# Kernel tuning notes

Hardware: AMD Instinct MI355X
Metric: run time of the kernel (lower is better)

The kernel has to match this reference:

```python
import jax, jax.numpy as jnp
import numpy as np

DIM = 1024
HEADS = 16
DIM_HEAD = 64
INNER = HEADS * DIM_HEAD  # 1024
SCALE = DIM_HEAD ** -0.5


def setup_inputs() -> dict:
    key = jax.random.key(0)
    ks = jax.random.split(key, 6)
    b, n = 4, 2048
    x = jax.random.normal(ks[0], (b, n, DIM), dtype=jnp.float32)
    gamma = jnp.ones((DIM,), dtype=jnp.float32)
    # weights stored (in, out); torch Linear computes x @ W.T with W (out, in)
    w_q = jax.random.normal(ks[1], (DIM, INNER), dtype=jnp.float32) * (DIM ** -0.5)
    w_kv = jax.random.normal(ks[2], (DIM, 2 * INNER), dtype=jnp.float32) * (DIM ** -0.5)
    w_out = jax.random.normal(ks[3], (INNER, DIM), dtype=jnp.float32) * (INNER ** -0.5)
    null_kv = jax.random.normal(ks[4], (2, HEADS, 1, DIM_HEAD), dtype=jnp.float32)
    return {"x": x, "gamma": gamma, "w_q": w_q, "w_kv": w_kv, "w_out": w_out, "null_kv": null_kv}


def _layer_norm(x, gamma):
    mu = jnp.mean(x, axis=-1, keepdims=True)
    var = jnp.var(x, axis=-1, keepdims=True)
    return (x - mu) * jax.lax.rsqrt(var + 1e-5) * gamma  # beta == 0


def reference(x, gamma, w_q, w_kv, w_out, null_kv):
    b, n, _ = x.shape
    xn = _layer_norm(x, gamma)
    q = xn @ w_q  # [b, n, inner]
    kv = xn @ w_kv
    k, v = jnp.split(kv, 2, axis=-1)
    q = q * SCALE

    def to_heads(t):
        return t.reshape(b, n, HEADS, DIM_HEAD).transpose(0, 2, 1, 3)  # b h n d

    q, k, v = map(to_heads, (q, k, v))
    nk = jnp.broadcast_to(null_kv[0][None], (b, HEADS, 1, DIM_HEAD))
    nv = jnp.broadcast_to(null_kv[1][None], (b, HEADS, 1, DIM_HEAD))
    k = jnp.concatenate([nk, k], axis=2)  # b h (n+1) d
    v = jnp.concatenate([nv, v], axis=2)
    sim = jnp.einsum('bhid,bhjd->bhij', q, k)
    attn = jax.nn.softmax(sim, axis=-1)
    out = jnp.einsum('bhij,bhjd->bhid', attn, v)
    out = out.transpose(0, 2, 1, 3).reshape(b, n, INNER)
    return out @ w_out
```

## Files before the change

### kernel.cpp

```cpp
#include <hip/hip_runtime.h>

typedef unsigned short ushort_t;
using f32x4   = __attribute__((ext_vector_type(4))) float;
using f32x16  = __attribute__((ext_vector_type(16))) float;
using bf16x8  = __attribute__((ext_vector_type(8))) __bf16;

typedef __attribute__((address_space(1))) const void gvoid_t;
typedef __attribute__((address_space(3))) void svoid_t;

union Frag {
    uint4    u4;
    bf16x8   b;
    ushort_t s[8];
};

__device__ __forceinline__ ushort_t f2bf(float f) {
    union { float f; unsigned u; } a; a.f = f;
    unsigned u = a.u;
    unsigned r = (u + 0x7fffu + ((u >> 16) & 1u)) >> 16;
    return (ushort_t)r;
}
__device__ __forceinline__ float bf2f(ushort_t b) {
    union { unsigned u; float f; } a; a.u = ((unsigned)b) << 16;
    return a.f;
}
__device__ __forceinline__ unsigned pack2bf(float lo, float hi) {
    union { __bf16 h[2]; unsigned u; } p;
    p.h[0] = (__bf16)lo;
    p.h[1] = (__bf16)hi;
    return p.u;
}
__device__ __forceinline__ float exp2_fast(float x) {
#if __has_builtin(__builtin_amdgcn_exp2f)
    return __builtin_amdgcn_exp2f(x);
#else
    return exp2f(x);
#endif
}
__device__ __forceinline__ void pl32swap(unsigned &x, unsigned &y) {
#if __has_builtin(__builtin_amdgcn_permlane32_swap)
    auto r = __builtin_amdgcn_permlane32_swap((int)x, (int)y, false, false);
    x = (unsigned)r[0]; y = (unsigned)r[1];
#else
    asm volatile("v_permlane32_swap_b32 %0, %1" : "+v"(x), "+v"(y));
#endif
}
__device__ __forceinline__ f32x16 mfma32(bf16x8 a, bf16x8 b, f32x16 c) {
    return __builtin_amdgcn_mfma_f32_32x32x16_bf16(a, b, c, 0, 0, 0);
}

#define QSCALE 0.18033688011112042f

__global__ __launch_bounds__(256)
void ln_kernel(const float* __restrict__ x, const float* __restrict__ gamma,
               ushort_t* __restrict__ xn)
{
    const int row = blockIdx.x;
    const int tid = threadIdx.x;
    const float4 v = *reinterpret_cast<const float4*>(x + (size_t)row * 1024 + tid * 4);

    float s = v.x + v.y + v.z + v.w;
    float q = v.x * v.x + v.y * v.y + v.z * v.z + v.w * v.w;
    #pragma unroll
    for (int off = 1; off <= 32; off <<= 1) {
        s += __shfl_xor(s, off);
        q += __shfl_xor(q, off);
    }
    __shared__ float ss[4], sq[4];
    if ((tid & 63) == 0) { ss[tid >> 6] = s; sq[tid >> 6] = q; }
    __syncthreads();
    const float S  = ss[0] + ss[1] + ss[2] + ss[3];
    const float Q  = sq[0] + sq[1] + sq[2] + sq[3];
    const float mu = S * (1.0f / 1024.0f);
    const float var = Q * (1.0f / 1024.0f) - mu * mu;
    const float rstd = rsqrtf(var + 1e-5f);

    const float4 gm = *reinterpret_cast<const float4*>(gamma + tid * 4);
    ushort4 o;
    o.x = f2bf((v.x - mu) * rstd * gm.x);
    o.y = f2bf((v.y - mu) * rstd * gm.y);
    o.z = f2bf((v.z - mu) * rstd * gm.z);
    o.w = f2bf((v.w - mu) * rstd * gm.w);
    *reinterpret_cast<ushort4*>(xn + (size_t)row * 1024 + tid * 4) = o;
}

__global__ __launch_bounds__(256)
void wt_kernel(const float* __restrict__ w, ushort_t* __restrict__ wt, int K, int N)
{
    __shared__ float tile[32][33];
    const int n0 = blockIdx.x * 32, k0 = blockIdx.y * 32;
    const int tx = threadIdx.x, ty = threadIdx.y;
    #pragma unroll
    for (int i = 0; i < 4; ++i) {
        int r = ty + i * 8;
        tile[r][tx] = w[(size_t)(k0 + r) * N + n0 + tx];
    }
    __syncthreads();
    #pragma unroll
    for (int i = 0; i < 4; ++i) {
        int r = ty + i * 8;
        wt[(size_t)(n0 + r) * K + k0 + tx] = f2bf(tile[tx][r]);
    }
}

template<int MODE>
__global__ __launch_bounds__(256)
void gemm_kernel(const ushort_t* __restrict__ A, const ushort_t* __restrict__ Bt,
                 ushort_t* __restrict__ o16a, ushort_t* __restrict__ o16b,
                 float* __restrict__ o32)
{
    __shared__ ushort_t ldsA[128 * 64];
    __shared__ ushort_t ldsB[128 * 64];

    const int tid = threadIdx.x;
    const int m0 = blockIdx.x * 128, n0 = blockIdx.y * 128;
    const int w = tid >> 6, l = tid & 63, g = l >> 4, c = l & 15;
    const int wm = w >> 1, wn = w & 1;

    const ushort_t* asrc[4];
    const ushort_t* bsrc[4];
    #pragma unroll
    for (int j = 0; j < 4; ++j) {
        const int gidx = j * 256 + tid;
        const int row = gidx >> 3;
        const int sl  = (gidx & 7) ^ (row & 7);
        asrc[j] = A  + (size_t)(m0 + row) * 1024 + sl * 8;
        bsrc[j] = Bt + (size_t)(n0 + row) * 1024 + sl * 8;
    }

    f32x4 acc[4][4];
    #pragma unroll
    for (int mi = 0; mi < 4; ++mi)
        #pragma unroll
        for (int ni = 0; ni < 4; ++ni)
            acc[mi][ni] = (f32x4){0.f, 0.f, 0.f, 0.f};

    const int swz = c & 7;

    for (int kt = 0; kt < 16; ++kt) {
        if (kt) __syncthreads();
        #pragma unroll
        for (int j = 0; j < 4; ++j) {
            __builtin_amdgcn_global_load_lds((gvoid_t*)(asrc[j] + kt * 64),
                                             (svoid_t*)(&ldsA[(j * 256 + tid) * 8]), 16, 0, 0);
            __builtin_amdgcn_global_load_lds((gvoid_t*)(bsrc[j] + kt * 64),
                                             (svoid_t*)(&ldsB[(j * 256 + tid) * 8]), 16, 0, 0);
        }
        __syncthreads();

        #pragma unroll
        for (int kk = 0; kk < 2; ++kk) {
            Frag af[4], bfr[4];
            #pragma unroll
            for (int mi = 0; mi < 4; ++mi)
                af[mi].u4 = *reinterpret_cast<const uint4*>(
                    &ldsA[(wm * 64 + mi * 16 + c) * 64 + ((((kk << 2) | g)) ^ swz) * 8]);
            #pragma unroll
            for (int ni = 0; ni < 4; ++ni)
                bfr[ni].u4 = *reinterpret_cast<const uint4*>(
                    &ldsB[(wn * 64 + ni * 16 + c) * 64 + ((((kk << 2) | g)) ^ swz) * 8]);
            #pragma unroll
            for (int mi = 0; mi < 4; ++mi)
                #pragma unroll
                for (int ni = 0; ni < 4; ++ni)
                    acc[mi][ni] = __builtin_amdgcn_mfma_f32_16x16x32_bf16(
                        af[mi].b, bfr[ni].b, acc[mi][ni], 0, 0, 0);
        }
    }

    #pragma unroll
    for (int mi = 0; mi < 4; ++mi) {
        const int mbase = m0 + wm * 64 + mi * 16 + g * 4;
        #pragma unroll
        for (int ni = 0; ni < 4; ++ni) {
            const int n = n0 + wn * 64 + ni * 16 + c;
            if (MODE == 0) {
                const int hh = n >> 6, d = n & 63;
                #pragma unroll
                for (int r = 0; r < 4; ++r) {
                    const int m = mbase + r;
                    const int b = m >> 11, tok = m & 2047;
                    o16a[(((size_t)b * 16 + hh) * 2048 + tok) * 64 + d] =
                        f2bf(acc[mi][ni][r] * QSCALE);
                }
            } else if (MODE == 1) {
                if (n < 1024) {
                    const int hh = n >> 6, d = n & 63;
                    #pragma unroll
                    for (int r = 0; r < 4; ++r) {
                        const int m = mbase + r;
                        const int b = m >> 11, tok = m & 2047;
                        o16a[(((size_t)b * 16 + hh) * 2048 + tok) * 64 + d] =
                            f2bf(acc[mi][ni][r]);
                    }
                } else {
                    const int nn = n - 1024;
                    const int hh = nn >> 6, d = nn & 63;
                    const int b = mbase >> 11, tok0 = mbase & 2047;
                    ushort4 pv;
                    pv.x = f2bf(acc[mi][ni][0]);
                    pv.y = f2bf(acc[mi][ni][1]);
                    pv.z = f2bf(acc[mi][ni][2]);
                    pv.w = f2bf(acc[mi][ni][3]);
                    *reinterpret_cast<ushort4*>(
                        o16b + (((size_t)b * 16 + hh) * 64 + d) * 2048 + tok0) = pv;
                }
            } else {
                #pragma unroll
                for (int r = 0; r < 4; ++r)
                    o32[(size_t)(mbase + r) * 1024 + n] = acc[mi][ni][r];
            }
        }
    }
}

__global__ __launch_bounds__(512)
void attn_kernel(const ushort_t* __restrict__ q, const ushort_t* __restrict__ k,
                 const ushort_t* __restrict__ vt, const float* __restrict__ nkv,
                 ushort_t* __restrict__ out)
{
    __shared__ ushort_t kvs[2][8192];

    const int tid = threadIdx.x;
    const int w = tid >> 6, l = tid & 63;
    const int qc = l & 31, hh = l >> 5;
    const int bh = blockIdx.x, qb = blockIdx.y, hd = bh & 15;

    const ushort_t* kb = k  + (size_t)bh * 2048 * 64;
    const ushort_t* vb = vt + (size_t)bh * 64 * 2048;

    const int srow = tid >> 3;
    const int ssl  = (tid & 7) ^ (srow & 7);
    const ushort_t* ksrc = kb + srow * 64 + ssl * 8;
    const ushort_t* vsrc = vb + srow * 2048 + ssl * 8;

    const ushort_t* qbase = q + ((size_t)bh * 2048 + qb * 256 + w * 32 + qc) * 64;
    Frag aq[4];
    #pragma unroll
    for (int dwin = 0; dwin < 4; ++dwin)
        aq[dwin].u4 = *reinterpret_cast<const uint4*>(qbase + dwin * 16 + hh * 8);

    float snull = 0.f;
    #pragma unroll
    for (int dwin = 0; dwin < 4; ++dwin) {
        const float4 n0 = *reinterpret_cast<const float4*>(nkv + hd * 64 + dwin * 16 + hh * 8);
        const float4 n1 = *reinterpret_cast<const float4*>(nkv + hd * 64 + dwin * 16 + hh * 8 + 4);
        snull += bf2f(aq[dwin].s[0]) * n0.x + bf2f(aq[dwin].s[1]) * n0.y
               + bf2f(aq[dwin].s[2]) * n0.z + bf2f(aq[dwin].s[3]) * n0.w;
        snull += bf2f(aq[dwin].s[4]) * n1.x + bf2f(aq[dwin].s[5]) * n1.y
               + bf2f(aq[dwin].s[6]) * n1.z + bf2f(aq[dwin].s[7]) * n1.w;
    }
    snull += __shfl_xor(snull, 32);

    float m_run  = snull;
    float l_part = (hh == 0) ? 1.f : 0.f;

    f32x16 acc[2];
    #pragma unroll
    for (int db = 0; db < 2; ++db)
        #pragma unroll
        for (int r = 0; r < 16; ++r)
            acc[db][r] = nkv[1024 + hd * 64 + db * 32 + (r & 3) + 8 * (r >> 2) + 4 * hh];

    const int swz = l & 7;

    __builtin_amdgcn_global_load_lds((gvoid_t*)(ksrc), (svoid_t*)(&kvs[0][tid * 8]), 16, 0, 0);
    __builtin_amdgcn_global_load_lds((gvoid_t*)(vsrc), (svoid_t*)(&kvs[0][4096 + tid * 8]), 16, 0, 0);
    __syncthreads();

    int cur = 0;
    for (int t = 0; t < 32; ++t) {
        if (t < 31) {
            __builtin_amdgcn_global_load_lds((gvoid_t*)(ksrc + (t + 1) * 4096),
                                             (svoid_t*)(&kvs[cur ^ 1][tid * 8]), 16, 0, 0);
            __builtin_amdgcn_global_load_lds((gvoid_t*)(vsrc + (t + 1) * 64),
                                             (svoid_t*)(&kvs[cur ^ 1][4096 + tid * 8]), 16, 0, 0);
        }
        const ushort_t* kbuf = &kvs[cur][0];
        const ushort_t* vbuf = &kvs[cur][4096];

        f32x16 st[2];
        __builtin_amdgcn_s_setprio(1);
        #pragma unroll
        for (int kvblk = 0; kvblk < 2; ++kvblk) {
            f32x16 z = {0.f,0.f,0.f,0.f, 0.f,0.f,0.f,0.f, 0.f,0.f,0.f,0.f, 0.f,0.f,0.f,0.f};
            #pragma unroll
            for (int dwin = 0; dwin < 4; ++dwin) {
                Frag kf;
                kf.u4 = *reinterpret_cast<const uint4*>(
                    &kbuf[(kvblk * 32 + (l & 31)) * 64 + (((dwin << 1) | hh) ^ swz) * 8]);
                z = mfma32(kf.b, aq[dwin].b, z);
            }
            st[kvblk] = z;
        }
        __builtin_amdgcn_s_setprio(0);

        float pm = st[0][0];
        #pragma unroll
        for (int r = 1; r < 16; ++r) pm = fmaxf(pm, st[0][r]);
        #pragma unroll
        for (int r = 0; r < 16; ++r) pm = fmaxf(pm, st[1][r]);
        pm = fmaxf(pm, __shfl_xor(pm, 32));

        if (__any(pm > m_run + 12.f)) {
            const float nm = fmaxf(m_run, pm);
            const float alpha = exp2_fast(m_run - nm);
            m_run = nm;
            l_part *= alpha;
            #pragma unroll
            for (int db = 0; db < 2; ++db)
                #pragma unroll
                for (int r = 0; r < 16; ++r)
                    acc[db][r] *= alpha;
        }

        float ts = 0.f;
        #pragma unroll
        for (int B = 0; B < 2; ++B)
            #pragma unroll
            for (int r = 0; r < 16; ++r) {
                st[B][r] = exp2_fast(st[B][r] - m_run);
                ts += st[B][r];
            }
        l_part += ts;

        Frag pb[2][2];
        #pragma unroll
        for (int B = 0; B < 2; ++B)
            #pragma unroll
            for (int kbv = 0; kbv < 2; ++kbv) {
                unsigned P = pack2bf(st[B][8 * kbv + 0], st[B][8 * kbv + 1]);
                unsigned Q = pack2bf(st[B][8 * kbv + 2], st[B][8 * kbv + 3]);
                unsigned R = pack2bf(st[B][8 * kbv + 4], st[B][8 * kbv + 5]);
                unsigned S = pack2bf(st[B][8 * kbv + 6], st[B][8 * kbv + 7]);
                pl32swap(P, R);
                pl32swap(Q, S);
                pb[B][kbv].u4.x = P;
                pb[B][kbv].u4.y = Q;
                pb[B][kbv].u4.z = R;
                pb[B][kbv].u4.w = S;
            }

        __builtin_amdgcn_s_setprio(1);
        #pragma unroll
        for (int db = 0; db < 2; ++db)
            #pragma unroll
            for (int B = 0; B < 2; ++B)
                #pragma unroll
                for (int kbv = 0; kbv < 2; ++kbv) {
                    Frag vf;
                    vf.u4 = *reinterpret_cast<const uint4*>(
                        &vbuf[(db * 32 + (l & 31)) * 64 + (((B << 2) | (kbv << 1) | hh) ^ swz) * 8]);
                    acc[db] = mfma32(vf.b, pb[B][kbv].b, acc[db]);
                }
        __builtin_amdgcn_s_setprio(0);

        __syncthreads();
        cur ^= 1;
    }

    l_part += __shfl_xor(l_part, 32);
    const float inv = 1.f / l_part;

    ushort_t* olds = &kvs[0][0];
    const int rowq = w * 32 + qc;
    #pragma unroll
    for (int db = 0; db < 2; ++db)
        #pragma unroll
        for (int rq = 0; rq < 4; ++rq) {
            uint2 ov;
            ov.x = pack2bf(acc[db][4 * rq + 0] * inv, acc[db][4 * rq + 1] * inv);
            ov.y = pack2bf(acc[db][4 * rq + 2] * inv, acc[db][4 * rq + 3] * inv);
            const int gL = db * 4 + rq;
            const int phys = gL ^ (qc & 7);
            *reinterpret_cast<uint2*>(&olds[(rowq * 8 + phys) * 8 + 4 * hh]) = ov;
        }
    __syncthreads();

    const size_t obase = ((size_t)(bh >> 4) * 2048 + qb * 256) * 1024 + hd * 64;
    #pragma unroll
    for (int p = 0; p < 4; ++p) {
        const int G = p * 512 + tid;
        const int row = G >> 3, sl = G & 7;
        const int phys = sl ^ (row & 7);
        uint4 v = *reinterpret_cast<const uint4*>(&olds[(row * 8 + phys) * 8]);
        *reinterpret_cast<uint4*>(out + obase + (size_t)row * 1024 + sl * 8) = v;
    }
}

extern "C" void kernel_launch(void* const* d_in, const int* in_sizes, int n_in,
                              void* d_out, int out_size, void* d_ws, size_t ws_size,
                              hipStream_t stream)
{
    (void)in_sizes; (void)n_in; (void)out_size; (void)ws_size;
    const float* x     = (const float*)d_in[0];
    const float* gamma = (const float*)d_in[1];
    const float* w_q   = (const float*)d_in[2];
    const float* w_kv  = (const float*)d_in[3];
    const float* w_out = (const float*)d_in[4];
    const float* nkv   = (const float*)d_in[5];
    float* out = (float*)d_out;

    char* ws = (char*)d_ws;
    ushort_t* xn   = (ushort_t*)(ws);
    ushort_t* wqT  = (ushort_t*)(ws + 16777216);
    ushort_t* wkvT = (ushort_t*)(ws + 18874368);
    ushort_t* woT  = (ushort_t*)(ws + 23068672);
    ushort_t* qh   = (ushort_t*)(ws + 25165824);
    ushort_t* kh   = (ushort_t*)(ws + 41943040);
    ushort_t* vtb  = (ushort_t*)(ws + 58720256);
    ushort_t* ao   = xn;

    ln_kernel<<<dim3(8192), dim3(256), 0, stream>>>(x, gamma, xn);
    wt_kernel<<<dim3(32, 32), dim3(32, 8), 0, stream>>>(w_q,  wqT, 1024, 1024);
    wt_kernel<<<dim3(64, 32), dim3(32, 8), 0, stream>>>(w_kv, wkvT, 1024, 2048);
    wt_kernel<<<dim3(32, 32), dim3(32, 8), 0, stream>>>(w_out, woT, 1024, 1024);

    gemm_kernel<0><<<dim3(64, 8),  dim3(256), 0, stream>>>(xn, wqT,  qh, nullptr, nullptr);
    gemm_kernel<1><<<dim3(64, 16), dim3(256), 0, stream>>>(xn, wkvT, kh, vtb, nullptr);

    attn_kernel<<<dim3(64, 8), dim3(512), 0, stream>>>(qh, kh, vtb, nkv, ao);

    gemm_kernel<2><<<dim3(64, 8), dim3(256), 0, stream>>>(ao, woT, nullptr, nullptr, out);
}
```

Baseline: 211.2 us.

## Fuse Q/KV projections, double-buffer GEMM LDS, shrink attention blocks to 256 threads

Result: slower. 224.7 us (+6.4%).

```diff
diff --git a/kernel.cpp b/kernel.cpp
--- a/kernel.cpp
+++ b/kernel.cpp
@@ -36,6 +36,9 @@
 #else
     return exp2f(x);
 #endif
+}
+__device__ __forceinline__ float fmax3(float a, float b, float c) {
+    return fmaxf(fmaxf(a, b), c);
 }
 __device__ __forceinline__ void pl32swap(unsigned &x, unsigned &y) {
 #if __has_builtin(__builtin_amdgcn_permlane32_swap)
@@ -103,14 +106,51 @@
     }
 }
 
+__device__ __forceinline__ void gemm_stage(const ushort_t* const* asrc,
+                                           const ushort_t* const* bsrc,
+                                           ushort_t* dA, ushort_t* dB,
+                                           int kt, int tid)
+{
+    #pragma unroll
+    for (int j = 0; j < 4; ++j) {
+        __builtin_amdgcn_global_load_lds((gvoid_t*)(asrc[j] + kt * 64),
+                                         (svoid_t*)(&dA[(j * 256 + tid) * 8]), 16, 0, 0);
+        __builtin_amdgcn_global_load_lds((gvoid_t*)(bsrc[j] + kt * 64),
+                                         (svoid_t*)(&dB[(j * 256 + tid) * 8]), 16, 0, 0);
+    }
+}
+__device__ __forceinline__ void gemm_comp(const ushort_t* bA, const ushort_t* bB,
+                                          f32x4 (&acc)[4][4],
+                                          int wm, int wn, int g, int c, int swz)
+{
+    #pragma unroll
+    for (int kk = 0; kk < 2; ++kk) {
+        Frag af[4], bfr[4];
+        #pragma unroll
+        for (int mi = 0; mi < 4; ++mi)
+            af[mi].u4 = *reinterpret_cast<const uint4*>(
+                &bA[(wm * 64 + mi * 16 + c) * 64 + ((((kk << 2) | g)) ^ swz) * 8]);
+        #pragma unroll
+        for (int ni = 0; ni < 4; ++ni)
+            bfr[ni].u4 = *reinterpret_cast<const uint4*>(
+                &bB[(wn * 64 + ni * 16 + c) * 64 + ((((kk << 2) | g)) ^ swz) * 8]);
+        #pragma unroll
+        for (int mi = 0; mi < 4; ++mi)
+            #pragma unroll
+            for (int ni = 0; ni < 4; ++ni)
+                acc[mi][ni] = __builtin_amdgcn_mfma_f32_16x16x32_bf16(
+                    af[mi].b, bfr[ni].b, acc[mi][ni], 0, 0, 0);
+    }
+}
+
 template<int MODE>
 __global__ __launch_bounds__(256)
 void gemm_kernel(const ushort_t* __restrict__ A, const ushort_t* __restrict__ Bt,
                  ushort_t* __restrict__ o16a, ushort_t* __restrict__ o16b,
                  float* __restrict__ o32)
 {
-    __shared__ ushort_t ldsA[128 * 64];
-    __shared__ ushort_t ldsB[128 * 64];
+    __shared__ ushort_t ldsA[2][128 * 64];
+    __shared__ ushort_t ldsB[2][128 * 64];
 
     const int tid = threadIdx.x;
     const int m0 = blockIdx.x * 128, n0 = blockIdx.y * 128;
@@ -137,35 +177,15 @@
 
     const int swz = c & 7;
 
-    for (int kt = 0; kt < 16; ++kt) {
-        if (kt) __syncthreads();
-        #pragma unroll
-        for (int j = 0; j < 4; ++j) {
-            __builtin_amdgcn_global_load_lds((gvoid_t*)(asrc[j] + kt * 64),
-                                             (svoid_t*)(&ldsA[(j * 256 + tid) * 8]), 16, 0, 0);
-            __builtin_amdgcn_global_load_lds((gvoid_t*)(bsrc[j] + kt * 64),
-                                             (svoid_t*)(&ldsB[(j * 256 + tid) * 8]), 16, 0, 0);
-        }
+    gemm_stage(asrc, bsrc, ldsA[0], ldsB[0], 0, tid);
+    #pragma unroll 1
+    for (int k2 = 0; k2 < 8; ++k2) {
         __syncthreads();
-
-        #pragma unroll
-        for (int kk = 0; kk < 2; ++kk) {
-            Frag af[4], bfr[4];
-            #pragma unroll
-            for (int mi = 0; mi < 4; ++mi)
-                af[mi].u4 = *reinterpret_cast<const uint4*>(
-                    &ldsA[(wm * 64 + mi * 16 + c) * 64 + ((((kk << 2) | g)) ^ swz) * 8]);
-            #pragma unroll
-            for (int ni = 0; ni < 4; ++ni)
-                bfr[ni].u4 = *reinterpret_cast<const uint4*>(
-                    &ldsB[(wn * 64 + ni * 16 + c) * 64 + ((((kk << 2) | g)) ^ swz) * 8]);
-            #pragma unroll
-            for (int mi = 0; mi < 4; ++mi)
-                #pragma unroll
-                for (int ni = 0; ni < 4; ++ni)
-                    acc[mi][ni] = __builtin_amdgcn_mfma_f32_16x16x32_bf16(
-                        af[mi].b, bfr[ni].b, acc[mi][ni], 0, 0, 0);
-        }
+        gemm_stage(asrc, bsrc, ldsA[1], ldsB[1], 2 * k2 + 1, tid);
+        gemm_comp(ldsA[0], ldsB[0], acc, wm, wn, g, c, swz);
+        __syncthreads();
+        if (k2 < 7) gemm_stage(asrc, bsrc, ldsA[0], ldsB[0], 2 * k2 + 2, tid);
+        gemm_comp(ldsA[1], ldsB[1], acc, wm, wn, g, c, swz);
     }
 
     #pragma unroll
@@ -175,26 +195,20 @@
         for (int ni = 0; ni < 4; ++ni) {
             const int n = n0 + wn * 64 + ni * 16 + c;
             if (MODE == 0) {
-                const int hh = n >> 6, d = n & 63;
-                #pragma unroll
-                for (int r = 0; r < 4; ++r) {
-                    const int m = mbase + r;
-                    const int b = m >> 11, tok = m & 2047;
-                    o16a[(((size_t)b * 16 + hh) * 2048 + tok) * 64 + d] =
-                        f2bf(acc[mi][ni][r] * QSCALE);
-                }
-            } else if (MODE == 1) {
-                if (n < 1024) {
-                    const int hh = n >> 6, d = n & 63;
+                if (n < 2048) {
+                    const int nn = n & 1023;
+                    const int hh = nn >> 6, d = nn & 63;
+                    const size_t base = (n < 1024) ? 0 : 8388608;
+                    const float scale = (n < 1024) ? QSCALE : 1.f;
                     #pragma unroll
                     for (int r = 0; r < 4; ++r) {
                         const int m = mbase + r;
                         const int b = m >> 11, tok = m & 2047;
-                        o16a[(((size_t)b * 16 + hh) * 2048 + tok) * 64 + d] =
-                            f2bf(acc[mi][ni][r]);
+                        o16a[base + (((size_t)b * 16 + hh) * 2048 + tok) * 64 + d] =
+                            f2bf(acc[mi][ni][r] * scale);
                     }
                 } else {
-                    const int nn = n - 1024;
+                    const int nn = n - 2048;
                     const int hh = nn >> 6, d = nn & 63;
                     const int b = mbase >> 11, tok0 = mbase & 2047;
                     ushort4 pv;
@@ -214,7 +228,7 @@
     }
 }
 
-__global__ __launch_bounds__(512)
+__global__ __launch_bounds__(256)
 void attn_kernel(const ushort_t* __restrict__ q, const ushort_t* __restrict__ k,
                  const ushort_t* __restrict__ vt, const float* __restrict__ nkv,
                  ushort_t* __restrict__ out)
@@ -231,10 +245,24 @@
 
     const int srow = tid >> 3;
     const int ssl  = (tid & 7) ^ (srow & 7);
-    const ushort_t* ksrc = kb + srow * 64 + ssl * 8;
-    const ushort_t* vsrc = vb + srow * 2048 + ssl * 8;
-
-    const ushort_t* qbase = q + ((size_t)bh * 2048 + qb * 256 + w * 32 + qc) * 64;
+    const ushort_t* ksrc0 = kb + srow * 64 + ssl * 8;
+    const ushort_t* vsrc0 = vb + srow * 2048 + ssl * 8;
+    const ushort_t* ksrc1 = ksrc0 + 32 * 64;
+    const ushort_t* vsrc1 = vsrc0 + 32 * 2048;
+
+#define ATTN_STAGE(BUF, T)                                                              \
+    do {                                                                                \
+        __builtin_amdgcn_global_load_lds((gvoid_t*)(ksrc0 + (T) * 4096),                \
+            (svoid_t*)(&kvs[BUF][tid * 8]), 16, 0, 0);                                  \
+        __builtin_amdgcn_global_load_lds((gvoid_t*)(ksrc1 + (T) * 4096),                \
+            (svoid_t*)(&kvs[BUF][(tid + 256) * 8]), 16, 0, 0);                          \
+        __builtin_amdgcn_global_load_lds((gvoid_t*)(vsrc0 + (T) * 64),                  \
+            (svoid_t*)(&kvs[BUF][4096 + tid * 8]), 16, 0, 0);                           \
+        __builtin_amdgcn_global_load_lds((gvoid_t*)(vsrc1 + (T) * 64),                  \
+            (svoid_t*)(&kvs[BUF][4096 + (tid + 256) * 8]), 16, 0, 0);                   \
+    } while (0)
+
+    const ushort_t* qbase = q + ((size_t)bh * 2048 + qb * 128 + w * 32 + qc) * 64;
     Frag aq[4];
     #pragma unroll
     for (int dwin = 0; dwin < 4; ++dwin)
@@ -264,104 +292,104 @@
 
     const int swz = l & 7;
 
-    __builtin_amdgcn_global_load_lds((gvoid_t*)(ksrc), (svoid_t*)(&kvs[0][tid * 8]), 16, 0, 0);
-    __builtin_amdgcn_global_load_lds((gvoid_t*)(vsrc), (svoid_t*)(&kvs[0][4096 + tid * 8]), 16, 0, 0);
-    __syncthreads();
-
-    int cur = 0;
-    for (int t = 0; t < 32; ++t) {
-        if (t < 31) {
-            __builtin_amdgcn_global_load_lds((gvoid_t*)(ksrc + (t + 1) * 4096),
-                                             (svoid_t*)(&kvs[cur ^ 1][tid * 8]), 16, 0, 0);
-            __builtin_amdgcn_global_load_lds((gvoid_t*)(vsrc + (t + 1) * 64),
-                                             (svoid_t*)(&kvs[cur ^ 1][4096 + tid * 8]), 16, 0, 0);
-        }
-        const ushort_t* kbuf = &kvs[cur][0];
-        const ushort_t* vbuf = &kvs[cur][4096];
-
-        f32x16 st[2];
-        __builtin_amdgcn_s_setprio(1);
-        #pragma unroll
-        for (int kvblk = 0; kvblk < 2; ++kvblk) {
-            f32x16 z = {0.f,0.f,0.f,0.f, 0.f,0.f,0.f,0.f, 0.f,0.f,0.f,0.f, 0.f,0.f,0.f,0.f};
-            #pragma unroll
-            for (int dwin = 0; dwin < 4; ++dwin) {
-                Frag kf;
-                kf.u4 = *reinterpret_cast<const uint4*>(
-                    &kbuf[(kvblk * 32 + (l & 31)) * 64 + (((dwin << 1) | hh) ^ swz) * 8]);
-                z = mfma32(kf.b, aq[dwin].b, z);
-            }
-            st[kvblk] = z;
-        }
-        __builtin_amdgcn_s_setprio(0);
-
-        float pm = st[0][0];
-        #pragma unroll
-        for (int r = 1; r < 16; ++r) pm = fmaxf(pm, st[0][r]);
-        #pragma unroll
-        for (int r = 0; r < 16; ++r) pm = fmaxf(pm, st[1][r]);
-        pm = fmaxf(pm, __shfl_xor(pm, 32));
-
-        if (__any(pm > m_run + 12.f)) {
-            const float nm = fmaxf(m_run, pm);
-            const float alpha = exp2_fast(m_run - nm);
-            m_run = nm;
-            l_part *= alpha;
-            #pragma unroll
-            for (int db = 0; db < 2; ++db)
-                #pragma unroll
-                for (int r = 0; r < 16; ++r)
-                    acc[db][r] *= alpha;
-        }
-
-        float ts = 0.f;
-        #pragma unroll
-        for (int B = 0; B < 2; ++B)
-            #pragma unroll
-            for (int r = 0; r < 16; ++r) {
-                st[B][r] = exp2_fast(st[B][r] - m_run);
-                ts += st[B][r];
-            }
-        l_part += ts;
-
-        Frag pb[2][2];
-        #pragma unroll
-        for (int B = 0; B < 2; ++B)
-            #pragma unroll
-            for (int kbv = 0; kbv < 2; ++kbv) {
-                unsigned P = pack2bf(st[B][8 * kbv + 0], st[B][8 * kbv + 1]);
-                unsigned Q = pack2bf(st[B][8 * kbv + 2], st[B][8 * kbv + 3]);
-                unsigned R = pack2bf(st[B][8 * kbv + 4], st[B][8 * kbv + 5]);
-                unsigned S = pack2bf(st[B][8 * kbv + 6], st[B][8 * kbv + 7]);
-                pl32swap(P, R);
-                pl32swap(Q, S);
-                pb[B][kbv].u4.x = P;
-                pb[B][kbv].u4.y = Q;
-                pb[B][kbv].u4.z = R;
-                pb[B][kbv].u4.w = S;
-            }
-
-        __builtin_amdgcn_s_setprio(1);
-        #pragma unroll
-        for (int db = 0; db < 2; ++db)
-            #pragma unroll
-            for (int B = 0; B < 2; ++B)
-                #pragma unroll
-                for (int kbv = 0; kbv < 2; ++kbv) {
-                    Frag vf;
-                    vf.u4 = *reinterpret_cast<const uint4*>(
-                        &vbuf[(db * 32 + (l & 31)) * 64 + (((B << 2) | (kbv << 1) | hh) ^ swz) * 8]);
-                    acc[db] = mfma32(vf.b, pb[B][kbv].b, acc[db]);
-                }
-        __builtin_amdgcn_s_setprio(0);
-
+#define ATTN_PROC(BUF)                                                                  \
+    do {                                                                                \
+        const ushort_t* kbuf = &kvs[BUF][0];                                            \
+        const ushort_t* vbuf = &kvs[BUF][4096];                                         \
+        f32x16 st[2];                                                                   \
+        __builtin_amdgcn_s_setprio(1);                                                  \
+        _Pragma("unroll")                                                               \
+        for (int kvblk = 0; kvblk < 2; ++kvblk) {                                       \
+            f32x16 z = {0.f,0.f,0.f,0.f,0.f,0.f,0.f,0.f,                                \
+                        0.f,0.f,0.f,0.f,0.f,0.f,0.f,0.f};                               \
+            _Pragma("unroll")                                                           \
+            for (int dwin = 0; dwin < 4; ++dwin) {                                      \
+                Frag kf;                                                                \
+                kf.u4 = *reinterpret_cast<const uint4*>(                                \
+                    &kbuf[(kvblk * 32 + qc) * 64 + (((dwin << 1) | hh) ^ swz) * 8]);    \
+                z = mfma32(kf.b, aq[dwin].b, z);                                        \
+            }                                                                           \
+            st[kvblk] = z;                                                              \
+        }                                                                               \
+        __builtin_amdgcn_s_setprio(0);                                                  \
+        float ch[4];                                                                    \
+        _Pragma("unroll")                                                               \
+        for (int j = 0; j < 4; ++j) {                                                   \
+            const int B = j >> 1, base = (j & 1) * 8;                                   \
+            ch[j] = fmaxf(st[B][base], st[B][base + 1]);                                \
+            ch[j] = fmax3(ch[j], st[B][base + 2], st[B][base + 3]);                     \
+            ch[j] = fmax3(ch[j], st[B][base + 4], st[B][base + 5]);                     \
+            ch[j] = fmax3(ch[j], st[B][base + 6], st[B][base + 7]);                     \
+        }                                                                               \
+        float pm = fmaxf(fmax3(ch[0], ch[1], ch[2]), ch[3]);                            \
+        pm = fmaxf(pm, __shfl_xor(pm, 32));                                             \
+        if (__any(pm > m_run + 12.f)) {                                                 \
+            const float nm = fmaxf(m_run, pm);                                          \
+            const float alpha = exp2_fast(m_run - nm);                                  \
+            m_run = nm;                                                                 \
+            l_part *= alpha;                                                            \
+            _Pragma("unroll")                                                           \
+            for (int db = 0; db < 2; ++db)                                              \
+                _Pragma("unroll")                                                       \
+                for (int r = 0; r < 16; ++r)                                            \
+                    acc[db][r] *= alpha;                                                \
+        }                                                                               \
+        float ts = 0.f;                                                                 \
+        _Pragma("unroll")                                                               \
+        for (int B = 0; B < 2; ++B)                                                     \
+            _Pragma("unroll")                                                           \
+            for (int r = 0; r < 16; ++r) {                                              \
+                st[B][r] = exp2_fast(st[B][r] - m_run);                                 \
+                ts += st[B][r];                                                         \
+            }                                                                           \
+        l_part += ts;                                                                   \
+        Frag pb[2][2];                                                                  \
+        _Pragma("unroll")                                                               \
+        for (int B = 0; B < 2; ++B)                                                     \
+            _Pragma("unroll")                                                           \
+            for (int kbv = 0; kbv < 2; ++kbv) {                                         \
+                unsigned P = pack2bf(st[B][8 * kbv + 0], st[B][8 * kbv + 1]);           \
+                unsigned Q = pack2bf(st[B][8 * kbv + 2], st[B][8 * kbv + 3]);           \
+                unsigned R = pack2bf(st[B][8 * kbv + 4], st[B][8 * kbv + 5]);           \
+                unsigned S = pack2bf(st[B][8 * kbv + 6], st[B][8 * kbv + 7]);           \
+                pl32swap(P, R);                                                         \
+                pl32swap(Q, S);                                                         \
+                pb[B][kbv].u4.x = P;                                                    \
+                pb[B][kbv].u4.y = Q;                                                    \
+                pb[B][kbv].u4.z = R;                                                    \
+                pb[B][kbv].u4.w = S;                                                    \
+            }                                                                           \
+        __builtin_amdgcn_s_setprio(1);                                                  \
+        _Pragma("unroll")                                                               \
+        for (int db = 0; db < 2; ++db)                                                  \
+            _Pragma("unroll")                                                           \
+            for (int B = 0; B < 2; ++B)                                                 \
+                _Pragma("unroll")                                                       \
+                for (int kbv = 0; kbv < 2; ++kbv) {                                     \
+                    Frag vf;                                                            \
+                    vf.u4 = *reinterpret_cast<const uint4*>(                            \
+                        &vbuf[(db * 32 + qc) * 64 +                                     \
+                              (((B << 2) | (kbv << 1) | hh) ^ swz) * 8]);               \
+                    acc[db] = mfma32(vf.b, pb[B][kbv].b, acc[db]);                      \
+                }                                                                       \
+        __builtin_amdgcn_s_setprio(0);                                                  \
+    } while (0)
+
+    ATTN_STAGE(0, 0);
+    #pragma unroll 1
+    for (int tt = 0; tt < 16; ++tt) {
         __syncthreads();
-        cur ^= 1;
+        ATTN_STAGE(1, 2 * tt + 1);
+        ATTN_PROC(0);
+        __syncthreads();
+        if (tt < 15) ATTN_STAGE(0, 2 * tt + 2);
+        ATTN_PROC(1);
     }
 
     l_part += __shfl_xor(l_part, 32);
     const float inv = 1.f / l_part;
 
+    __syncthreads();
     ushort_t* olds = &kvs[0][0];
     const int rowq = w * 32 + qc;
     #pragma unroll
@@ -377,15 +405,17 @@
         }
     __syncthreads();
 
-    const size_t obase = ((size_t)(bh >> 4) * 2048 + qb * 256) * 1024 + hd * 64;
+    const size_t obase = ((size_t)(bh >> 4) * 2048 + qb * 128) * 1024 + hd * 64;
     #pragma unroll
     for (int p = 0; p < 4; ++p) {
-        const int G = p * 512 + tid;
+        const int G = p * 256 + tid;
         const int row = G >> 3, sl = G & 7;
         const int phys = sl ^ (row & 7);
         uint4 v = *reinterpret_cast<const uint4*>(&olds[(row * 8 + phys) * 8]);
         *reinterpret_cast<uint4*>(out + obase + (size_t)row * 1024 + sl * 8) = v;
     }
+#undef ATTN_STAGE
+#undef ATTN_PROC
 }
 
 extern "C" void kernel_launch(void* const* d_in, const int* in_sizes, int n_in,
@@ -402,24 +432,22 @@
     float* out = (float*)d_out;
 
     char* ws = (char*)d_ws;
-    ushort_t* xn   = (ushort_t*)(ws);
-    ushort_t* wqT  = (ushort_t*)(ws + 16777216);
-    ushort_t* wkvT = (ushort_t*)(ws + 18874368);
-    ushort_t* woT  = (ushort_t*)(ws + 23068672);
-    ushort_t* qh   = (ushort_t*)(ws + 25165824);
-    ushort_t* kh   = (ushort_t*)(ws + 41943040);
-    ushort_t* vtb  = (ushort_t*)(ws + 58720256);
-    ushort_t* ao   = xn;
+    ushort_t* xn    = (ushort_t*)(ws);
+    ushort_t* wqkvT = (ushort_t*)(ws + 16777216);
+    ushort_t* woT   = (ushort_t*)(ws + 23068672);
+    ushort_t* qh    = (ushort_t*)(ws + 25165824);
+    ushort_t* vtb   = (ushort_t*)(ws + 58720256);
+    ushort_t* ao    = xn;
+    ushort_t* kh    = qh + 8388608;
 
     ln_kernel<<<dim3(8192), dim3(256), 0, stream>>>(x, gamma, xn);
-    wt_kernel<<<dim3(32, 32), dim3(32, 8), 0, stream>>>(w_q,  wqT, 1024, 1024);
-    wt_kernel<<<dim3(64, 32), dim3(32, 8), 0, stream>>>(w_kv, wkvT, 1024, 2048);
+    wt_kernel<<<dim3(32, 32), dim3(32, 8), 0, stream>>>(w_q,  wqkvT, 1024, 1024);
+    wt_kernel<<<dim3(64, 32), dim3(32, 8), 0, stream>>>(w_kv, wqkvT + 1048576, 1024, 2048);
     wt_kernel<<<dim3(32, 32), dim3(32, 8), 0, stream>>>(w_out, woT, 1024, 1024);
 
-    gemm_kernel<0><<<dim3(64, 8),  dim3(256), 0, stream>>>(xn, wqT,  qh, nullptr, nullptr);
-    gemm_kernel<1><<<dim3(64, 16), dim3(256), 0, stream>>>(xn, wkvT, kh, vtb, nullptr);
-
-    attn_kernel<<<dim3(64, 8), dim3(512), 0, stream>>>(qh, kh, vtb, nkv, ao);
+    gemm_kernel<0><<<dim3(64, 24), dim3(256), 0, stream>>>(xn, wqkvT, qh, vtb, nullptr);
+
+    attn_kernel<<<dim3(64, 16), dim3(256), 0, stream>>>(qh, kh, vtb, nkv, ao);
 
     gemm_kernel<2><<<dim3(64, 8), dim3(256), 0, stream>>>(ao, woT, nullptr, nullptr, out);
 }
```

## Double-buffer GEMM LDS, fuse QKV GEMMs, and process two query tiles per attention wave

Applied to the files above, without the earlier changes.

Measured after the change: 209.4 us. Within noise of the previous version (-0.9%).

```diff
diff --git a/kernel.cpp b/kernel.cpp
--- a/kernel.cpp
+++ b/kernel.cpp
@@ -36,6 +36,9 @@
 #else
     return exp2f(x);
 #endif
+}
+__device__ __forceinline__ float fmax3(float a, float b, float c) {
+    return fmaxf(fmaxf(a, b), c);
 }
 __device__ __forceinline__ void pl32swap(unsigned &x, unsigned &y) {
 #if __has_builtin(__builtin_amdgcn_permlane32_swap)
@@ -103,14 +106,51 @@
     }
 }
 
+__device__ __forceinline__ void gemm_stage(const ushort_t* const* asrc,
+                                           const ushort_t* const* bsrc,
+                                           ushort_t* dA, ushort_t* dB,
+                                           int kt, int tid)
+{
+    #pragma unroll
+    for (int j = 0; j < 4; ++j) {
+        __builtin_amdgcn_global_load_lds((gvoid_t*)(asrc[j] + kt * 64),
+                                         (svoid_t*)(&dA[(j * 256 + tid) * 8]), 16, 0, 0);
+        __builtin_amdgcn_global_load_lds((gvoid_t*)(bsrc[j] + kt * 64),
+                                         (svoid_t*)(&dB[(j * 256 + tid) * 8]), 16, 0, 0);
+    }
+}
+__device__ __forceinline__ void gemm_comp(const ushort_t* bA, const ushort_t* bB,
+                                          f32x4 (&acc)[4][4],
+                                          int wm, int wn, int g, int c, int swz)
+{
+    #pragma unroll
+    for (int kk = 0; kk < 2; ++kk) {
+        Frag af[4], bfr[4];
+        #pragma unroll
+        for (int mi = 0; mi < 4; ++mi)
+            af[mi].u4 = *reinterpret_cast<const uint4*>(
+                &bA[(wm * 64 + mi * 16 + c) * 64 + ((((kk << 2) | g)) ^ swz) * 8]);
+        #pragma unroll
+        for (int ni = 0; ni < 4; ++ni)
+            bfr[ni].u4 = *reinterpret_cast<const uint4*>(
+                &bB[(wn * 64 + ni * 16 + c) * 64 + ((((kk << 2) | g)) ^ swz) * 8]);
+        #pragma unroll
+        for (int mi = 0; mi < 4; ++mi)
+            #pragma unroll
+            for (int ni = 0; ni < 4; ++ni)
+                acc[mi][ni] = __builtin_amdgcn_mfma_f32_16x16x32_bf16(
+                    af[mi].b, bfr[ni].b, acc[mi][ni], 0, 0, 0);
+    }
+}
+
 template<int MODE>
 __global__ __launch_bounds__(256)
 void gemm_kernel(const ushort_t* __restrict__ A, const ushort_t* __restrict__ Bt,
                  ushort_t* __restrict__ o16a, ushort_t* __restrict__ o16b,
                  float* __restrict__ o32)
 {
-    __shared__ ushort_t ldsA[128 * 64];
-    __shared__ ushort_t ldsB[128 * 64];
+    __shared__ ushort_t ldsA[2][128 * 64];
+    __shared__ ushort_t ldsB[2][128 * 64];
 
     const int tid = threadIdx.x;
     const int m0 = blockIdx.x * 128, n0 = blockIdx.y * 128;
@@ -137,35 +177,15 @@
 
     const int swz = c & 7;
 
-    for (int kt = 0; kt < 16; ++kt) {
-        if (kt) __syncthreads();
-        #pragma unroll
-        for (int j = 0; j < 4; ++j) {
-            __builtin_amdgcn_global_load_lds((gvoid_t*)(asrc[j] + kt * 64),
-                                             (svoid_t*)(&ldsA[(j * 256 + tid) * 8]), 16, 0, 0);
-            __builtin_amdgcn_global_load_lds((gvoid_t*)(bsrc[j] + kt * 64),
-                                             (svoid_t*)(&ldsB[(j * 256 + tid) * 8]), 16, 0, 0);
-        }
+    gemm_stage(asrc, bsrc, ldsA[0], ldsB[0], 0, tid);
+    #pragma unroll 1
+    for (int k2 = 0; k2 < 8; ++k2) {
         __syncthreads();
-
-        #pragma unroll
-        for (int kk = 0; kk < 2; ++kk) {
-            Frag af[4], bfr[4];
-            #pragma unroll
-            for (int mi = 0; mi < 4; ++mi)
-                af[mi].u4 = *reinterpret_cast<const uint4*>(
-                    &ldsA[(wm * 64 + mi * 16 + c) * 64 + ((((kk << 2) | g)) ^ swz) * 8]);
-            #pragma unroll
-            for (int ni = 0; ni < 4; ++ni)
-                bfr[ni].u4 = *reinterpret_cast<const uint4*>(
-                    &ldsB[(wn * 64 + ni * 16 + c) * 64 + ((((kk << 2) | g)) ^ swz) * 8]);
-            #pragma unroll
-            for (int mi = 0; mi < 4; ++mi)
-                #pragma unroll
-                for (int ni = 0; ni < 4; ++ni)
-                    acc[mi][ni] = __builtin_amdgcn_mfma_f32_16x16x32_bf16(
-                        af[mi].b, bfr[ni].b, acc[mi][ni], 0, 0, 0);
-        }
+        gemm_stage(asrc, bsrc, ldsA[1], ldsB[1], 2 * k2 + 1, tid);
+        gemm_comp(ldsA[0], ldsB[0], acc, wm, wn, g, c, swz);
+        __syncthreads();
+        if (k2 < 7) gemm_stage(asrc, bsrc, ldsA[0], ldsB[0], 2 * k2 + 2, tid);
+        gemm_comp(ldsA[1], ldsB[1], acc, wm, wn, g, c, swz);
     }
 
     #pragma unroll
@@ -175,26 +195,20 @@
         for (int ni = 0; ni < 4; ++ni) {
             const int n = n0 + wn * 64 + ni * 16 + c;
             if (MODE == 0) {
-                const int hh = n >> 6, d = n & 63;
-                #pragma unroll
-                for (int r = 0; r < 4; ++r) {
-                    const int m = mbase + r;
-                    const int b = m >> 11, tok = m & 2047;
-                    o16a[(((size_t)b * 16 + hh) * 2048 + tok) * 64 + d] =
-                        f2bf(acc[mi][ni][r] * QSCALE);
-                }
-            } else if (MODE == 1) {
-                if (n < 1024) {
-                    const int hh = n >> 6, d = n & 63;
+                if (n < 2048) {
+                    const int nn = n & 1023;
+                    const int hh = nn >> 6, d = nn & 63;
+                    const size_t base = (n < 1024) ? 0 : 8388608;
+                    const float scale = (n < 1024) ? QSCALE : 1.f;
                     #pragma unroll
                     for (int r = 0; r < 4; ++r) {
                         const int m = mbase + r;
                         const int b = m >> 11, tok = m & 2047;
-                        o16a[(((size_t)b * 16 + hh) * 2048 + tok) * 64 + d] =
-                            f2bf(acc[mi][ni][r]);
+                        o16a[base + (((size_t)b * 16 + hh) * 2048 + tok) * 64 + d] =
+                            f2bf(acc[mi][ni][r] * scale);
                     }
                 } else {
-                    const int nn = n - 1024;
+                    const int nn = n - 2048;
                     const int hh = nn >> 6, d = nn & 63;
                     const int b = mbase >> 11, tok0 = mbase & 2047;
                     ushort4 pv;
@@ -234,33 +248,43 @@
     const ushort_t* ksrc = kb + srow * 64 + ssl * 8;
     const ushort_t* vsrc = vb + srow * 2048 + ssl * 8;
 
-    const ushort_t* qbase = q + ((size_t)bh * 2048 + qb * 256 + w * 32 + qc) * 64;
-    Frag aq[4];
-    #pragma unroll
-    for (int dwin = 0; dwin < 4; ++dwin)
-        aq[dwin].u4 = *reinterpret_cast<const uint4*>(qbase + dwin * 16 + hh * 8);
-
-    float snull = 0.f;
-    #pragma unroll
-    for (int dwin = 0; dwin < 4; ++dwin) {
-        const float4 n0 = *reinterpret_cast<const float4*>(nkv + hd * 64 + dwin * 16 + hh * 8);
-        const float4 n1 = *reinterpret_cast<const float4*>(nkv + hd * 64 + dwin * 16 + hh * 8 + 4);
-        snull += bf2f(aq[dwin].s[0]) * n0.x + bf2f(aq[dwin].s[1]) * n0.y
-               + bf2f(aq[dwin].s[2]) * n0.z + bf2f(aq[dwin].s[3]) * n0.w;
-        snull += bf2f(aq[dwin].s[4]) * n1.x + bf2f(aq[dwin].s[5]) * n1.y
-               + bf2f(aq[dwin].s[6]) * n1.z + bf2f(aq[dwin].s[7]) * n1.w;
-    }
-    snull += __shfl_xor(snull, 32);
-
-    float m_run  = snull;
-    float l_part = (hh == 0) ? 1.f : 0.f;
-
-    f32x16 acc[2];
-    #pragma unroll
-    for (int db = 0; db < 2; ++db)
+    const ushort_t* qbase = q + ((size_t)bh * 2048 + qb * 512 + w * 64 + qc) * 64;
+    Frag aq[2][4];
+    #pragma unroll
+    for (int j = 0; j < 2; ++j)
+        #pragma unroll
+        for (int dwin = 0; dwin < 4; ++dwin)
+            aq[j][dwin].u4 = *reinterpret_cast<const uint4*>(
+                qbase + j * 32 * 64 + dwin * 16 + hh * 8);
+
+    float m_run[2], l_part[2];
+    #pragma unroll
+    for (int j = 0; j < 2; ++j) {
+        float sn = 0.f;
+        #pragma unroll
+        for (int dwin = 0; dwin < 4; ++dwin) {
+            const float4 n0 = *reinterpret_cast<const float4*>(nkv + hd * 64 + dwin * 16 + hh * 8);
+            const float4 n1 = *reinterpret_cast<const float4*>(nkv + hd * 64 + dwin * 16 + hh * 8 + 4);
+            sn += bf2f(aq[j][dwin].s[0]) * n0.x + bf2f(aq[j][dwin].s[1]) * n0.y
+                + bf2f(aq[j][dwin].s[2]) * n0.z + bf2f(aq[j][dwin].s[3]) * n0.w;
+            sn += bf2f(aq[j][dwin].s[4]) * n1.x + bf2f(aq[j][dwin].s[5]) * n1.y
+                + bf2f(aq[j][dwin].s[6]) * n1.z + bf2f(aq[j][dwin].s[7]) * n1.w;
+        }
+        sn += __shfl_xor(sn, 32);
+        m_run[j]  = sn;
+        l_part[j] = (hh == 0) ? 1.f : 0.f;
+    }
+
+    f32x16 acc[2][2];
+    #pragma unroll
+    for (int db = 0; db < 2; ++db) {
+        f32x16 tmp;
         #pragma unroll
         for (int r = 0; r < 16; ++r)
-            acc[db][r] = nkv[1024 + hd * 64 + db * 32 + (r & 3) + 8 * (r >> 2) + 4 * hh];
+            tmp[r] = nkv[1024 + hd * 64 + db * 32 + (r & 3) + 8 * (r >> 2) + 4 * hh];
+        acc[0][db] = tmp;
+        acc[1][db] = tmp;
+    }
 
     const int swz = l & 7;
 
@@ -269,6 +293,7 @@
     __syncthreads();
 
     int cur = 0;
+    #pragma unroll 1
     for (int t = 0; t < 32; ++t) {
         if (t < 31) {
             __builtin_amdgcn_global_load_lds((gvoid_t*)(ksrc + (t + 1) * 4096),
@@ -279,67 +304,86 @@
         const ushort_t* kbuf = &kvs[cur][0];
         const ushort_t* vbuf = &kvs[cur][4096];
 
-        f32x16 st[2];
+        f32x16 st[2][2];
+        #pragma unroll
+        for (int j = 0; j < 2; ++j)
+            #pragma unroll
+            for (int kvblk = 0; kvblk < 2; ++kvblk)
+                st[j][kvblk] = (f32x16){0.f,0.f,0.f,0.f,0.f,0.f,0.f,0.f,
+                                        0.f,0.f,0.f,0.f,0.f,0.f,0.f,0.f};
         __builtin_amdgcn_s_setprio(1);
         #pragma unroll
-        for (int kvblk = 0; kvblk < 2; ++kvblk) {
-            f32x16 z = {0.f,0.f,0.f,0.f, 0.f,0.f,0.f,0.f, 0.f,0.f,0.f,0.f, 0.f,0.f,0.f,0.f};
+        for (int kvblk = 0; kvblk < 2; ++kvblk)
             #pragma unroll
             for (int dwin = 0; dwin < 4; ++dwin) {
                 Frag kf;
                 kf.u4 = *reinterpret_cast<const uint4*>(
-                    &kbuf[(kvblk * 32 + (l & 31)) * 64 + (((dwin << 1) | hh) ^ swz) * 8]);
-                z = mfma32(kf.b, aq[dwin].b, z);
+                    &kbuf[(kvblk * 32 + qc) * 64 + (((dwin << 1) | hh) ^ swz) * 8]);
+                st[0][kvblk] = mfma32(kf.b, aq[0][dwin].b, st[0][kvblk]);
+                st[1][kvblk] = mfma32(kf.b, aq[1][dwin].b, st[1][kvblk]);
             }
-            st[kvblk] = z;
-        }
         __builtin_amdgcn_s_setprio(0);
 
-        float pm = st[0][0];
-        #pragma unroll
-        for (int r = 1; r < 16; ++r) pm = fmaxf(pm, st[0][r]);
-        #pragma unroll
-        for (int r = 0; r < 16; ++r) pm = fmaxf(pm, st[1][r]);
-        pm = fmaxf(pm, __shfl_xor(pm, 32));
-
-        if (__any(pm > m_run + 12.f)) {
-            const float nm = fmaxf(m_run, pm);
-            const float alpha = exp2_fast(m_run - nm);
-            m_run = nm;
-            l_part *= alpha;
-            #pragma unroll
-            for (int db = 0; db < 2; ++db)
+        float pm[2];
+        #pragma unroll
+        for (int j = 0; j < 2; ++j) {
+            float ch[4];
+            #pragma unroll
+            for (int jj = 0; jj < 4; ++jj) {
+                const int B = jj >> 1, base = (jj & 1) * 8;
+                ch[jj] = fmaxf(st[j][B][base], st[j][B][base + 1]);
+                ch[jj] = fmax3(ch[jj], st[j][B][base + 2], st[j][B][base + 3]);
+                ch[jj] = fmax3(ch[jj], st[j][B][base + 4], st[j][B][base + 5]);
+                ch[jj] = fmax3(ch[jj], st[j][B][base + 6], st[j][B][base + 7]);
+            }
+            float pmv = fmaxf(fmax3(ch[0], ch[1], ch[2]), ch[3]);
+            pmv = fmaxf(pmv, __shfl_xor(pmv, 32));
+            pm[j] = pmv;
+        }
+
+        if (__any(fmaxf(pm[0] - m_run[0], pm[1] - m_run[1]) > 12.f)) {
+            #pragma unroll
+            for (int j = 0; j < 2; ++j) {
+                const float nm = fmaxf(m_run[j], pm[j]);
+                const float alpha = exp2_fast(m_run[j] - nm);
+                m_run[j] = nm;
+                l_part[j] *= alpha;
                 #pragma unroll
-                for (int r = 0; r < 16; ++r)
-                    acc[db][r] *= alpha;
-        }
-
-        float ts = 0.f;
-        #pragma unroll
-        for (int B = 0; B < 2; ++B)
-            #pragma unroll
-            for (int r = 0; r < 16; ++r) {
-                st[B][r] = exp2_fast(st[B][r] - m_run);
-                ts += st[B][r];
+                for (int db = 0; db < 2; ++db)
+                    #pragma unroll
+                    for (int r = 0; r < 16; ++r)
+                        acc[j][db][r] *= alpha;
             }
-        l_part += ts;
-
-        Frag pb[2][2];
-        #pragma unroll
-        for (int B = 0; B < 2; ++B)
-            #pragma unroll
-            for (int kbv = 0; kbv < 2; ++kbv) {
-                unsigned P = pack2bf(st[B][8 * kbv + 0], st[B][8 * kbv + 1]);
-                unsigned Q = pack2bf(st[B][8 * kbv + 2], st[B][8 * kbv + 3]);
-                unsigned R = pack2bf(st[B][8 * kbv + 4], st[B][8 * kbv + 5]);
-                unsigned S = pack2bf(st[B][8 * kbv + 6], st[B][8 * kbv + 7]);
-                pl32swap(P, R);
-                pl32swap(Q, S);
-                pb[B][kbv].u4.x = P;
-                pb[B][kbv].u4.y = Q;
-                pb[B][kbv].u4.z = R;
-                pb[B][kbv].u4.w = S;
-            }
+        }
+
+        Frag pb[2][2][2];
+        #pragma unroll
+        for (int j = 0; j < 2; ++j) {
+            float ts = 0.f;
+            #pragma unroll
+            for (int B = 0; B < 2; ++B)
+                #pragma unroll
+                for (int r = 0; r < 16; ++r) {
+                    st[j][B][r] = exp2_fast(st[j][B][r] - m_run[j]);
+                    ts += st[j][B][r];
+                }
+            l_part[j] += ts;
+            #pragma unroll
+            for (int B = 0; B < 2; ++B)
+                #pragma unroll
+                for (int kbv = 0; kbv < 2; ++kbv) {
+                    unsigned P = pack2bf(st[j][B][8 * kbv + 0], st[j][B][8 * kbv + 1]);
+                    unsigned Q = pack2bf(st[j][B][8 * kbv + 2], st[j][B][8 * kbv + 3]);
+                    unsigned R = pack2bf(st[j][B][8 * kbv + 4], st[j][B][8 * kbv + 5]);
+                    unsigned S = pack2bf(st[j][B][8 * kbv + 6], st[j][B][8 * kbv + 7]);
+                    pl32swap(P, R);
+                    pl32swap(Q, S);
+                    pb[j][B][kbv].u4.x = P;
+                    pb[j][B][kbv].u4.y = Q;
+                    pb[j][B][kbv].u4.z = R;
+                    pb[j][B][kbv].u4.w = S;
+                }
+        }
 
         __builtin_amdgcn_s_setprio(1);
         #pragma unroll
@@ -350,8 +394,10 @@
                 for (int kbv = 0; kbv < 2; ++kbv) {
                     Frag vf;
                     vf.u4 = *reinterpret_cast<const uint4*>(
-                        &vbuf[(db * 32 + (l & 31)) * 64 + (((B << 2) | (kbv << 1) | hh) ^ swz) * 8]);
-                    acc[db] = mfma32(vf.b, pb[B][kbv].b, acc[db]);
+                        &vbuf[(db * 32 + qc) * 64 +
+                              (((B << 2) | (kbv << 1) | hh) ^ swz) * 8]);
+                    acc[0][db] = mfma32(vf.b, pb[0][B][kbv].b, acc[0][db]);
+                    acc[1][db] = mfma32(vf.b, pb[1][B][kbv].b, acc[1][db]);
                 }
         __builtin_amdgcn_s_setprio(0);
 
@@ -359,32 +405,42 @@
         cur ^= 1;
     }
 
-    l_part += __shfl_xor(l_part, 32);
-    const float inv = 1.f / l_part;
+    float inv[2];
+    #pragma unroll
+    for (int j = 0; j < 2; ++j) {
+        l_part[j] += __shfl_xor(l_part[j], 32);
+        inv[j] = 1.f / l_part[j];
+    }
 
     ushort_t* olds = &kvs[0][0];
-    const int rowq = w * 32 + qc;
-    #pragma unroll
-    for (int db = 0; db < 2; ++db)
-        #pragma unroll
-        for (int rq = 0; rq < 4; ++rq) {
-            uint2 ov;
-            ov.x = pack2bf(acc[db][4 * rq + 0] * inv, acc[db][4 * rq + 1] * inv);
-            ov.y = pack2bf(acc[db][4 * rq + 2] * inv, acc[db][4 * rq + 3] * inv);
-            const int gL = db * 4 + rq;
-            const int phys = gL ^ (qc & 7);
-            *reinterpret_cast<uint2*>(&olds[(rowq * 8 + phys) * 8 + 4 * hh]) = ov;
-        }
-    __syncthreads();
-
-    const size_t obase = ((size_t)(bh >> 4) * 2048 + qb * 256) * 1024 + hd * 64;
-    #pragma unroll
-    for (int p = 0; p < 4; ++p) {
-        const int G = p * 512 + tid;
-        const int row = G >> 3, sl = G & 7;
-        const int phys = sl ^ (row & 7);
-        uint4 v = *reinterpret_cast<const uint4*>(&olds[(row * 8 + phys) * 8]);
-        *reinterpret_cast<uint4*>(out + obase + (size_t)row * 1024 + sl * 8) = v;
+    const size_t obase = ((size_t)(bh >> 4) * 2048) * 1024 + hd * 64;
+    #pragma unroll
+    for (int j = 0; j < 2; ++j) {
+        __syncthreads();
+        const int rowq = w * 32 + qc;
+        #pragma unroll
+        for (int db = 0; db < 2; ++db)
+            #pragma unroll
+            for (int rq = 0; rq < 4; ++rq) {
+                uint2 ov;
+                ov.x = pack2bf(acc[j][db][4 * rq + 0] * inv[j],
+                               acc[j][db][4 * rq + 1] * inv[j]);
+                ov.y = pack2bf(acc[j][db][4 * rq + 2] * inv[j],
+                               acc[j][db][4 * rq + 3] * inv[j]);
+                const int gL = db * 4 + rq;
+                const int phys = gL ^ (qc & 7);
+                *reinterpret_cast<uint2*>(&olds[(rowq * 8 + phys) * 8 + 4 * hh]) = ov;
+            }
+        __syncthreads();
+        #pragma unroll
+        for (int p = 0; p < 4; ++p) {
+            const int G = p * 512 + tid;
+            const int row = G >> 3, sl = G & 7;
+            const int phys = sl ^ (row & 7);
+            uint4 v = *reinterpret_cast<const uint4*>(&olds[(row * 8 + phys) * 8]);
+            const int gr = qb * 512 + (row >> 5) * 64 + j * 32 + (row & 31);
+            *reinterpret_cast<uint4*>(out + obase + (size_t)gr * 1024 + sl * 8) = v;
+        }
     }
 }
 
@@ -402,24 +458,22 @@
     float* out = (float*)d_out;
 
     char* ws = (char*)d_ws;
-    ushort_t* xn   = (ushort_t*)(ws);
-    ushort_t* wqT  = (ushort_t*)(ws + 16777216);
-    ushort_t* wkvT = (ushort_t*)(ws + 18874368);
-    ushort_t* woT  = (ushort_t*)(ws + 23068672);
-    ushort_t* qh   = (ushort_t*)(ws + 25165824);
-    ushort_t* kh   = (ushort_t*)(ws + 41943040);
-    ushort_t* vtb  = (ushort_t*)(ws + 58720256);
-    ushort_t* ao   = xn;
+    ushort_t* xn    = (ushort_t*)(ws);
+    ushort_t* wqkvT = (ushort_t*)(ws + 16777216);
+    ushort_t* woT   = (ushort_t*)(ws + 23068672);
+    ushort_t* qh    = (ushort_t*)(ws + 25165824);
+    ushort_t* vtb   = (ushort_t*)(ws + 58720256);
+    ushort_t* ao    = xn;
+    ushort_t* kh    = qh + 8388608;
 
     ln_kernel<<<dim3(8192), dim3(256), 0, stream>>>(x, gamma, xn);
-    wt_kernel<<<dim3(32, 32), dim3(32, 8), 0, stream>>>(w_q,  wqT, 1024, 1024);
-    wt_kernel<<<dim3(64, 32), dim3(32, 8), 0, stream>>>(w_kv, wkvT, 1024, 2048);
+    wt_kernel<<<dim3(32, 32), dim3(32, 8), 0, stream>>>(w_q,  wqkvT, 1024, 1024);
+    wt_kernel<<<dim3(64, 32), dim3(32, 8), 0, stream>>>(w_kv, wqkvT + 1048576, 1024, 2048);
     wt_kernel<<<dim3(32, 32), dim3(32, 8), 0, stream>>>(w_out, woT, 1024, 1024);
 
-    gemm_kernel<0><<<dim3(64, 8),  dim3(256), 0, stream>>>(xn, wqT,  qh, nullptr, nullptr);
-    gemm_kernel<1><<<dim3(64, 16), dim3(256), 0, stream>>>(xn, wkvT, kh, vtb, nullptr);
-
-    attn_kernel<<<dim3(64, 8), dim3(512), 0, stream>>>(qh, kh, vtb, nkv, ao);
+    gemm_kernel<0><<<dim3(64, 24), dim3(256), 0, stream>>>(xn, wqkvT, qh, vtb, nullptr);
+
+    attn_kernel<<<dim3(64, 4), dim3(512), 0, stream>>>(qh, kh, vtb, nkv, ao);
 
     gemm_kernel<2><<<dim3(64, 8), dim3(256), 0, stream>>>(ao, woT, nullptr, nullptr, out);
 }
```
